# Optimization experiments

Hardware: AMD Instinct MI355X
Metric: run time of the kernel (lower is better)

Reference implementation:

```python
import jax, jax.numpy as jnp
import numpy as np

N = 100000
E = 1600000
F_IN = 602
NHID = 128
N_CLS = 41


def setup_inputs() -> dict:
    key = jax.random.key(0)
    k1, k2, k3, k4 = jax.random.split(key, 4)
    x = jax.random.normal(k1, (N, F_IN), dtype=jnp.float32)
    edge_index = jax.random.randint(k2, (2, E), 0, N, dtype=jnp.int64)
    # Glorot-style scaled weights
    W1 = jax.random.normal(k3, (F_IN, NHID), dtype=jnp.float32) * (1.0 / np.sqrt(F_IN))
    b1 = jnp.zeros((NHID,), dtype=jnp.float32)
    W2 = jax.random.normal(k4, (NHID, N_CLS), dtype=jnp.float32) * (1.0 / np.sqrt(NHID))
    b2 = jnp.zeros((N_CLS,), dtype=jnp.float32)
    return {"x": x, "edge_index": edge_index, "W1": W1, "b1": b1, "W2": W2, "b2": b2}


def reference(x, edge_index, W1, b1, W2, b2):
    n = x.shape[0]
    loop = jnp.arange(n, dtype=edge_index.dtype)
    # PyG GCNConv: add self-loops, symmetric normalization D^-1/2 (A+I) D^-1/2
    src = jnp.concatenate([edge_index[0], loop])  # [E+N]
    dst = jnp.concatenate([edge_index[1], loop])  # [E+N]
    ones = jnp.ones(src.shape[0], dtype=x.dtype)
    deg = jax.ops.segment_sum(ones, dst, num_segments=n)  # in-degree incl self-loop
    dinv = jnp.where(deg > 0, jax.lax.rsqrt(deg), 0.0)
    norm = dinv[src] * dinv[dst]  # [E+N]

    def conv(h, W, b):
        h = h @ W  # transform first (smaller feature dim for gather)
        msg = h[src] * norm[:, None]  # gather + scale
        return jax.ops.segment_sum(msg, dst, num_segments=n) + b  # scatter-add

    h = jax.nn.relu(conv(x, W1, b1))
    # dropout is identity in eval mode
    out = conv(h, W2, b2)
    return jax.nn.log_softmax(out, axis=1)
```

## Files before the change

kernel.cpp:

```cpp
#include <hip/hip_runtime.h>
#include <math.h>

#define GK 602
#define GH 128
#define GC 41
#define GCP 48
#define KPAD 608
#define NKT 19
#define GS 40

typedef __bf16 bf16x8 __attribute__((ext_vector_type(8)));
typedef float f32x16 __attribute__((ext_vector_type(16)));

__device__ __forceinline__ unsigned short f2bf(float f) {
    __bf16 b = (__bf16)f;
    return __builtin_bit_cast(unsigned short, b);
}
__device__ __forceinline__ float bf2f(unsigned short u) {
    return __uint_as_float((unsigned int)u << 16);
}
__device__ __forceinline__ float bflo(unsigned int u) { return __uint_as_float(u << 16); }
__device__ __forceinline__ float bfhi(unsigned int u) { return __uint_as_float(u & 0xffff0000u); }


__global__ void k_hist(const int* __restrict__ dst, int* __restrict__ counts, int E) {
    int e = blockIdx.x * 256 + threadIdx.x;
    if (e < E) atomicAdd(&counts[dst[e]], 1);
}

__global__ void k_scan_a(const int* __restrict__ counts, int* __restrict__ row_ptr,
                         int* __restrict__ bsum, int n) {
    __shared__ int wsum[4];
    int t = threadIdx.x;
    int lane = t & 63;
    int wv = t >> 6;
    int base = blockIdx.x * 1024 + t * 4;
    int v[4];
    int s = 0;
#pragma unroll
    for (int j = 0; j < 4; ++j) {
        int idx = base + j;
        v[j] = (idx < n) ? counts[idx] : 0;
        s += v[j];
    }
    int incl = s;
#pragma unroll
    for (int o = 1; o < 64; o <<= 1) {
        int x = __shfl_up(incl, o);
        if (lane >= o) incl += x;
    }
    if (lane == 63) wsum[wv] = incl;
    __syncthreads();
    int woff = 0;
#pragma unroll
    for (int i = 0; i < 3; ++i) woff += (i < wv) ? wsum[i] : 0;
    if (t == 255) bsum[blockIdx.x] = woff + incl;
    int off = woff + incl - s;
#pragma unroll
    for (int j = 0; j < 4; ++j) {
        int idx = base + j;
        if (idx < n) row_ptr[idx] = off;
        off += v[j];
    }
}

__global__ void k_scan_b(int* __restrict__ bsum, int nb) {
    __shared__ int sh[256];
    int t = threadIdx.x;
    int v = (t < nb) ? bsum[t] : 0;
    sh[t] = v;
    __syncthreads();
    for (int o = 1; o < 256; o <<= 1) {
        int x = (t >= o) ? sh[t - o] : 0;
        __syncthreads();
        sh[t] += x;
        __syncthreads();
    }
    if (t < nb) bsum[t] = sh[t] - v;
}

__global__ void k_scan_c(int* __restrict__ row_ptr, const int* __restrict__ bsum,
                         const int* __restrict__ counts, float* __restrict__ dinv,
                         int* __restrict__ cursor, int n, int E) {
    int i = blockIdx.x * 256 + threadIdx.x;
    if (i < n) {
        int rp = row_ptr[i] + bsum[i >> 10];
        row_ptr[i] = rp;
        cursor[i] = rp;
        dinv[i] = rsqrtf((float)(counts[i] + 1));
    }
    if (i == 0) row_ptr[n] = E;
}

__global__ void k_fill(const int* __restrict__ src, const int* __restrict__ dst,
                       const float* __restrict__ dinv,
                       int* __restrict__ cursor, int2* __restrict__ meta, int E) {
    int e = blockIdx.x * 256 + threadIdx.x;
    if (e < E) {
        int s = src[e];
        int d = dst[e];
        int p = atomicAdd(&cursor[d], 1);
        float w = dinv[s] * dinv[d];
        meta[p] = make_int2(s, __float_as_int(w));
    }
}


__global__ void k_prepW1(const float* __restrict__ W1, unsigned short* __restrict__ W1T) {
    int i = blockIdx.x * 256 + threadIdx.x;
    if (i >= GH * KPAD) return;
    int n = i / KPAD;
    int k = i - n * KPAD;
    float v = (k < GK) ? W1[(size_t)k * GH + n] : 0.f;
    W1T[i] = f2bf(v);
}


struct AF { float4 v0, v1, v2, v3; };

__device__ __forceinline__ AF loadA(const float* __restrict__ xr, int kb, bool tail) {
    AF r;
    if (!tail) {
        r.v0 = *(const float4*)(xr + kb);
        r.v1 = *(const float4*)(xr + kb + 4);
        r.v2 = *(const float4*)(xr + kb + 16);
        r.v3 = *(const float4*)(xr + kb + 20);
    } else {
        float tv[8], tw[8];
#pragma unroll
        for (int j = 0; j < 8; ++j) {
            int k0_ = kb + j;
            int k1_ = kb + 16 + j;
            tv[j] = (k0_ < GK) ? xr[k0_] : 0.f;
            tw[j] = (k1_ < GK) ? xr[k1_] : 0.f;
        }
        r.v0 = make_float4(tv[0], tv[1], tv[2], tv[3]);
        r.v1 = make_float4(tv[4], tv[5], tv[6], tv[7]);
        r.v2 = make_float4(tw[0], tw[1], tw[2], tw[3]);
        r.v3 = make_float4(tw[4], tw[5], tw[6], tw[7]);
    }
    return r;
}

__device__ __forceinline__ bf16x8 cvt8(float4 a, float4 b) {
    bf16x8 r;
    r[0] = (__bf16)a.x; r[1] = (__bf16)a.y; r[2] = (__bf16)a.z; r[3] = (__bf16)a.w;
    r[4] = (__bf16)b.x; r[5] = (__bf16)b.y; r[6] = (__bf16)b.z; r[7] = (__bf16)b.w;
    return r;
}

__device__ __forceinline__ void stageB(const unsigned short* __restrict__ W1T,
                                       __bf16* __restrict__ Bsb, int tid, int k0) {
#pragma unroll
    for (int s = 0; s < 2; ++s) {
        int slot = tid + 256 * s;
        int n = slot >> 2;
        int j = slot & 3;
        uint4 v = *(const uint4*)&W1T[(size_t)n * KPAD + k0 + 8 * j];
        *(uint4*)&Bsb[n * GS + 8 * j] = v;
    }
}

__global__ __launch_bounds__(256) void k_gemm1_mfma(const float* __restrict__ X,
                                                    const unsigned short* __restrict__ W1T,
                                                    unsigned short* __restrict__ Y, int M) {
    __shared__ __bf16 Bs[2][128 * GS];
    int tid = threadIdx.x;
    int lane = tid & 63;
    int w = tid >> 6;
    int rowBase = blockIdx.x * 64 + (w & 1) * 32;
    int cg = w >> 1;
    int grow_base = rowBase + (lane & 31);
    int arow = (grow_base < M) ? grow_base : (M - 1);
    const float* xr = X + (size_t)arow * GK;
    int kh = (lane >> 5) * 8;
    int bn = lane & 31;

    f32x16 acc[2];
#pragma unroll
    for (int c = 0; c < 2; ++c)
#pragma unroll
        for (int i = 0; i < 16; ++i) acc[c][i] = 0.f;

    stageB(W1T, Bs[0], tid, 0);
    AF a = loadA(xr, kh, false);
    __syncthreads();

    int buf = 0;
    for (int it = 0; it < NKT; ++it) {
        AF an;
        if (it + 1 < NKT) {
            stageB(W1T, Bs[buf ^ 1], tid, 32 * (it + 1));
            an = loadA(xr, kh + 32 * (it + 1), (it + 1) == (NKT - 1));
        }
        bf16x8 af0 = cvt8(a.v0, a.v1);
        bf16x8 af1 = cvt8(a.v2, a.v3);
#pragma unroll
        for (int c = 0; c < 2; ++c) {
            int nt = 2 * cg + c;
            bf16x8 b0 = *(const bf16x8*)&Bs[buf][(32 * nt + bn) * GS + kh];
            acc[c] = __builtin_amdgcn_mfma_f32_32x32x16_bf16(af0, b0, acc[c], 0, 0, 0);
        }
#pragma unroll
        for (int c = 0; c < 2; ++c) {
            int nt = 2 * cg + c;
            bf16x8 b1 = *(const bf16x8*)&Bs[buf][(32 * nt + bn) * GS + 16 + kh];
            acc[c] = __builtin_amdgcn_mfma_f32_32x32x16_bf16(af1, b1, acc[c], 0, 0, 0);
        }
        __syncthreads();
        buf ^= 1;
        a = an;
    }
#pragma unroll
    for (int c = 0; c < 2; ++c) {
        int nt = 2 * cg + c;
#pragma unroll
        for (int reg = 0; reg < 16; ++reg) {
            int rrow = (reg & 3) + 8 * (reg >> 2) + 4 * (lane >> 5);
            int grow = rowBase + rrow;
            int gcol = 32 * nt + (lane & 31);
            if (grow < M) Y[(size_t)grow * GH + gcol] = f2bf(acc[c][reg]);
        }
    }
}


__global__ __launch_bounds__(256) void k_agg1(const unsigned int* __restrict__ H,
                                              unsigned int* __restrict__ O,
                                              const int* __restrict__ row_ptr,
                                              const int2* __restrict__ meta,
                                              const float* __restrict__ dinv,
                                              const float* __restrict__ bias, int n) {
    int wv = threadIdx.x >> 6;
    int lane = threadIdx.x & 63;
    int d = blockIdx.x * 4 + wv;
    if (d >= n) return;
    float dd = dinv[d];
    int beg = row_ptr[d], end = row_ptr[d + 1];
    unsigned int v = H[(size_t)d * 64 + lane];
    float sw = dd * dd;
    float a0 = sw * bflo(v);
    float a1 = sw * bfhi(v);
    int e = beg;
    for (; e + 16 <= end; e += 16) {
        int2 m[16];
        unsigned int u[16];
#pragma unroll
        for (int j = 0; j < 16; ++j) m[j] = meta[e + j];
#pragma unroll
        for (int j = 0; j < 16; ++j) u[j] = H[(size_t)m[j].x * 64 + lane];
#pragma unroll
        for (int j = 0; j < 16; ++j) {
            float wj = __int_as_float(m[j].y);
            a0 = fmaf(wj, bflo(u[j]), a0);
            a1 = fmaf(wj, bfhi(u[j]), a1);
        }
    }
    if (e + 8 <= end) {
        int2 m[8];
        unsigned int u[8];
#pragma unroll
        for (int j = 0; j < 8; ++j) m[j] = meta[e + j];
#pragma unroll
        for (int j = 0; j < 8; ++j) u[j] = H[(size_t)m[j].x * 64 + lane];
#pragma unroll
        for (int j = 0; j < 8; ++j) {
            float wj = __int_as_float(m[j].y);
            a0 = fmaf(wj, bflo(u[j]), a0);
            a1 = fmaf(wj, bfhi(u[j]), a1);
        }
        e += 8;
    }
    if (e + 4 <= end) {
        int2 m[4];
        unsigned int u[4];
#pragma unroll
        for (int j = 0; j < 4; ++j) m[j] = meta[e + j];
#pragma unroll
        for (int j = 0; j < 4; ++j) u[j] = H[(size_t)m[j].x * 64 + lane];
#pragma unroll
        for (int j = 0; j < 4; ++j) {
            float wj = __int_as_float(m[j].y);
            a0 = fmaf(wj, bflo(u[j]), a0);
            a1 = fmaf(wj, bfhi(u[j]), a1);
        }
        e += 4;
    }
    for (; e < end; ++e) {
        int2 m = meta[e];
        unsigned int u = H[(size_t)m.x * 64 + lane];
        float wj = __int_as_float(m.y);
        a0 = fmaf(wj, bflo(u), a0);
        a1 = fmaf(wj, bfhi(u), a1);
    }
    a0 = fmaxf(a0 + bias[2 * lane], 0.f);
    a1 = fmaxf(a1 + bias[2 * lane + 1], 0.f);
    O[(size_t)d * 64 + lane] = (unsigned int)f2bf(a0) | ((unsigned int)f2bf(a1) << 16);
}


__global__ __launch_bounds__(256) void k_gemm2t(const unsigned int* __restrict__ Hb,
                                                const float* __restrict__ W2,
                                                unsigned short* __restrict__ G, int n) {
    __shared__ float ws[128][GCP];
    for (int i = threadIdx.x; i < 128 * GCP; i += 256) {
        int k = i / GCP;
        int c = i - k * GCP;
        ws[k][c] = (c < GC) ? W2[k * GC + c] : 0.f;
    }
    __syncthreads();
    int r0 = blockIdx.x * 512 + threadIdx.x;
    int r1 = r0 + 256;
    bool v0 = r0 < n, v1 = r1 < n;
    float acc0[GCP], acc1[GCP];
#pragma unroll
    for (int c = 0; c < GCP; ++c) { acc0[c] = 0.f; acc1[c] = 0.f; }
    const uint2* h0 = (const uint2*)(Hb + (size_t)(v0 ? r0 : 0) * 64);
    const uint2* h1 = (const uint2*)(Hb + (size_t)(v1 ? r1 : 0) * 64);
    for (int q = 0; q < 32; ++q) {
        uint2 ua = h0[q];
        uint2 ub = h1[q];
        float va[4] = {bflo(ua.x), bfhi(ua.x), bflo(ua.y), bfhi(ua.y)};
        float vb[4] = {bflo(ub.x), bfhi(ub.x), bflo(ub.y), bfhi(ub.y)};
#pragma unroll
        for (int j = 0; j < 4; ++j) {
            int k = 4 * q + j;
#pragma unroll
            for (int cq = 0; cq < GCP / 4; ++cq) {
                float4 wv = *(const float4*)&ws[k][4 * cq];
                acc0[4 * cq + 0] = fmaf(va[j], wv.x, acc0[4 * cq + 0]);
                acc0[4 * cq + 1] = fmaf(va[j], wv.y, acc0[4 * cq + 1]);
                acc0[4 * cq + 2] = fmaf(va[j], wv.z, acc0[4 * cq + 2]);
                acc0[4 * cq + 3] = fmaf(va[j], wv.w, acc0[4 * cq + 3]);
                acc1[4 * cq + 0] = fmaf(vb[j], wv.x, acc1[4 * cq + 0]);
                acc1[4 * cq + 1] = fmaf(vb[j], wv.y, acc1[4 * cq + 1]);
                acc1[4 * cq + 2] = fmaf(vb[j], wv.z, acc1[4 * cq + 2]);
                acc1[4 * cq + 3] = fmaf(vb[j], wv.w, acc1[4 * cq + 3]);
            }
        }
    }
    if (v0) {
#pragma unroll
        for (int c = 0; c < GCP; ++c) G[(size_t)r0 * GCP + c] = f2bf(acc0[c]);
    }
    if (v1) {
#pragma unroll
        for (int c = 0; c < GCP; ++c) G[(size_t)r1 * GCP + c] = f2bf(acc1[c]);
    }
}


__global__ __launch_bounds__(256) void k_agg2(const unsigned short* __restrict__ G,
                                              float* __restrict__ out,
                                              const int* __restrict__ row_ptr,
                                              const int2* __restrict__ meta,
                                              const float* __restrict__ dinv,
                                              const float* __restrict__ b2, int n) {
    int wv = threadIdx.x >> 6;
    int lane = threadIdx.x & 63;
    int gl = (lane < GCP) ? lane : (GCP - 1);
    int d = blockIdx.x * 4 + wv;
    if (d >= n) return;
    float dd = dinv[d];
    int beg = row_ptr[d], end = row_ptr[d + 1];
    float a = dd * dd * bf2f(G[(size_t)d * GCP + gl]);
    int e = beg;
    for (; e + 16 <= end; e += 16) {
        int2 m[16];
        unsigned short u[16];
#pragma unroll
        for (int j = 0; j < 16; ++j) m[j] = meta[e + j];
#pragma unroll
        for (int j = 0; j < 16; ++j) u[j] = G[(size_t)m[j].x * GCP + gl];
#pragma unroll
        for (int j = 0; j < 16; ++j) a = fmaf(__int_as_float(m[j].y), bf2f(u[j]), a);
    }
    if (e + 8 <= end) {
        int2 m[8];
        unsigned short u[8];
#pragma unroll
        for (int j = 0; j < 8; ++j) m[j] = meta[e + j];
#pragma unroll
        for (int j = 0; j < 8; ++j) u[j] = G[(size_t)m[j].x * GCP + gl];
#pragma unroll
        for (int j = 0; j < 8; ++j) a = fmaf(__int_as_float(m[j].y), bf2f(u[j]), a);
        e += 8;
    }
    if (e + 4 <= end) {
        int2 m[4];
        unsigned short u[4];
#pragma unroll
        for (int j = 0; j < 4; ++j) m[j] = meta[e + j];
#pragma unroll
        for (int j = 0; j < 4; ++j) u[j] = G[(size_t)m[j].x * GCP + gl];
#pragma unroll
        for (int j = 0; j < 4; ++j) a = fmaf(__int_as_float(m[j].y), bf2f(u[j]), a);
        e += 4;
    }
    for (; e < end; ++e) {
        int2 m = meta[e];
        a = fmaf(__int_as_float(m.y), bf2f(G[(size_t)m.x * GCP + gl]), a);
    }
    float logit = (lane < GC) ? (a + b2[lane]) : -INFINITY;
    float mx = logit;
#pragma unroll
    for (int off = 32; off; off >>= 1) mx = fmaxf(mx, __shfl_xor(mx, off));
    float ex = (lane < GC) ? __expf(logit - mx) : 0.f;
    float sm = ex;
#pragma unroll
    for (int off = 32; off; off >>= 1) sm += __shfl_xor(sm, off);
    if (lane < GC) out[(size_t)d * GC + lane] = logit - mx - __logf(sm);
}


static inline size_t alignup256(size_t x) { return (x + 255) & ~(size_t)255; }

extern "C" void kernel_launch(void* const* d_in, const int* in_sizes, int n_in,
                              void* d_out, int out_size, void* d_ws, size_t ws_size,
                              hipStream_t stream) {
    const float* x  = (const float*)d_in[0];
    const int*   ei = (const int*)d_in[1];
    const float* W1 = (const float*)d_in[2];
    const float* b1 = (const float*)d_in[3];
    const float* W2 = (const float*)d_in[4];
    const float* b2 = (const float*)d_in[5];
    float* out = (float*)d_out;

    const int n = in_sizes[0] / GK;
    const int E = in_sizes[1] / 2;
    const int* src = ei;
    const int* dst = ei + E;

    char* w = (char*)d_ws;
    char* p;
    p = w; w += alignup256((size_t)n * 4);            float* dinv  = (float*)p;
    p = w; w += alignup256((size_t)n * 4);            int* counts  = (int*)p;
    p = w; w += alignup256((size_t)n * 4);            int* cursor  = (int*)p;
    p = w; w += alignup256((size_t)(n + 1) * 4);      int* row_ptr = (int*)p;
    p = w; w += alignup256(1024 * 4);                 int* bsum    = (int*)p;
    p = w; w += alignup256((size_t)E * 8);            int2* meta   = (int2*)p;
    p = w; w += alignup256((size_t)GH * KPAD * 2);    unsigned short* W1T = (unsigned short*)p;
    p = w; w += alignup256((size_t)n * GH * 2);       unsigned short* bufA = (unsigned short*)p;
    p = w; w += alignup256((size_t)n * GH * 2);       unsigned short* bufB = (unsigned short*)p;
    p = w; w += alignup256((size_t)n * GCP * 2);      unsigned short* G    = (unsigned short*)p;

    hipMemsetAsync(counts, 0, (size_t)n * 4, stream);

    int gE = (E + 255) / 256;
    int gN = (n + 255) / 256;
    int nb = (n + 1023) / 1024;

    k_hist<<<gE, 256, 0, stream>>>(dst, counts, E);
    k_scan_a<<<nb, 256, 0, stream>>>(counts, row_ptr, bsum, n);
    k_scan_b<<<1, 256, 0, stream>>>(bsum, nb);
    k_scan_c<<<gN, 256, 0, stream>>>(row_ptr, bsum, counts, dinv, cursor, n, E);
    k_fill<<<gE, 256, 0, stream>>>(src, dst, dinv, cursor, meta, E);

    k_prepW1<<<(GH * KPAD + 255) / 256, 256, 0, stream>>>(W1, W1T);
    k_gemm1_mfma<<<(n + 63) / 64, 256, 0, stream>>>(x, W1T, bufA, n);
    k_agg1<<<(n + 3) / 4, 256, 0, stream>>>((const unsigned int*)bufA, (unsigned int*)bufB,
                                            row_ptr, meta, dinv, b1, n);
    k_gemm2t<<<(n + 511) / 512, 256, 0, stream>>>((const unsigned int*)bufB, W2, G, n);
    k_agg2<<<(n + 3) / 4, 256, 0, stream>>>(G, out, row_ptr, meta, dinv, b2, n);
}
```

Before: 721.7 us.

## Restructure GEMM1: per-wave 32x128 tiles, fragment-packed W1 from global, LDS-staged coalesced X

The first-layer GEMM is reorganised so each wave computes a full 32-row by 128-column tile, making four MFMA accumulators and 128 rows per block. W1 is pre-packed into MFMA fragment order, so B operands are read straight from global memory (L2/L1-resident) instead of being staged through shared memory with barriers. X rows are loaded with coalesced float4 reads, converted to bf16 and written to a per-wave double-buffered LDS region, with no block-level syncs. The goal is to cut redundant X reads, LDS traffic and barrier stalls in the memory-bound X stream. In exchange it adds register pressure and depends on cache hits for the W1 fragments.

```diff
diff --git a/kernel.cpp b/kernel.cpp
--- a/kernel.cpp
+++ b/kernel.cpp
@@ -7,7 +7,6 @@
 #define GCP 48
 #define KPAD 608
 #define NKT 19
-#define GS 40
 
 typedef __bf16 bf16x8 __attribute__((ext_vector_type(8)));
 typedef float f32x16 __attribute__((ext_vector_type(16)));
@@ -106,122 +105,126 @@
 }
 
 
-__global__ void k_prepW1(const float* __restrict__ W1, unsigned short* __restrict__ W1T) {
+__global__ void k_prepW1F(const float* __restrict__ W1, unsigned short* __restrict__ W1F) {
     int i = blockIdx.x * 256 + threadIdx.x;
-    if (i >= GH * KPAD) return;
-    int n = i / KPAD;
-    int k = i - n * KPAD;
-    float v = (k < GK) ? W1[(size_t)k * GH + n] : 0.f;
-    W1T[i] = f2bf(v);
-}
-
-
-struct AF { float4 v0, v1, v2, v3; };
-
-__device__ __forceinline__ AF loadA(const float* __restrict__ xr, int kb, bool tail) {
-    AF r;
-    if (!tail) {
-        r.v0 = *(const float4*)(xr + kb);
-        r.v1 = *(const float4*)(xr + kb + 4);
-        r.v2 = *(const float4*)(xr + kb + 16);
-        r.v3 = *(const float4*)(xr + kb + 20);
-    } else {
-        float tv[8], tw[8];
-#pragma unroll
-        for (int j = 0; j < 8; ++j) {
-            int k0_ = kb + j;
-            int k1_ = kb + 16 + j;
-            tv[j] = (k0_ < GK) ? xr[k0_] : 0.f;
-            tw[j] = (k1_ < GK) ? xr[k1_] : 0.f;
-        }
-        r.v0 = make_float4(tv[0], tv[1], tv[2], tv[3]);
-        r.v1 = make_float4(tv[4], tv[5], tv[6], tv[7]);
-        r.v2 = make_float4(tw[0], tw[1], tw[2], tw[3]);
-        r.v3 = make_float4(tw[4], tw[5], tw[6], tw[7]);
-    }
-    return r;
-}
-
-__device__ __forceinline__ bf16x8 cvt8(float4 a, float4 b) {
-    bf16x8 r;
-    r[0] = (__bf16)a.x; r[1] = (__bf16)a.y; r[2] = (__bf16)a.z; r[3] = (__bf16)a.w;
-    r[4] = (__bf16)b.x; r[5] = (__bf16)b.y; r[6] = (__bf16)b.z; r[7] = (__bf16)b.w;
-    return r;
-}
-
-__device__ __forceinline__ void stageB(const unsigned short* __restrict__ W1T,
-                                       __bf16* __restrict__ Bsb, int tid, int k0) {
-#pragma unroll
-    for (int s = 0; s < 2; ++s) {
-        int slot = tid + 256 * s;
-        int n = slot >> 2;
-        int j = slot & 3;
-        uint4 v = *(const uint4*)&W1T[(size_t)n * KPAD + k0 + 8 * j];
-        *(uint4*)&Bsb[n * GS + 8 * j] = v;
-    }
-}
-
-__global__ __launch_bounds__(256) void k_gemm1_mfma(const float* __restrict__ X,
-                                                    const unsigned short* __restrict__ W1T,
-                                                    unsigned short* __restrict__ Y, int M) {
-    __shared__ __bf16 Bs[2][128 * GS];
+    if (i >= NKT * 4096) return;
+    int kt = i >> 12;
+    int r  = i & 4095;
+    int nt = r >> 10;
+    int r2 = r & 1023;
+    int bs = r2 >> 9;
+    int r3 = r2 & 511;
+    int ln = r3 >> 3;
+    int j  = r3 & 7;
+    int col = 32 * nt + (ln & 31);
+    int k   = 32 * kt + 16 * bs + 8 * (ln >> 5) + j;
+    float v = (k < GK) ? W1[(size_t)k * GH + col] : 0.f;
+    W1F[i] = f2bf(v);
+}
+
+
+__device__ __forceinline__ void issueA(const float* __restrict__ X, int rowBase,
+                                       int ro, int q, int kb, int M, float4* av) {
+#pragma unroll
+    for (int i = 0; i < 4; ++i) {
+        int r = rowBase + 8 * i + ro;
+        if (r >= M) r = M - 1;
+        const float* p = X + (size_t)r * GK + kb + 4 * q;
+        av[i] = *(const float4*)p;
+    }
+}
+
+__device__ __forceinline__ void issueA_tail(const float* __restrict__ X, int rowBase,
+                                            int ro, int q, int kb, int M, float4* av) {
+#pragma unroll
+    for (int i = 0; i < 4; ++i) {
+        int r = rowBase + 8 * i + ro;
+        if (r >= M) r = M - 1;
+        const float* p = X + (size_t)r * GK;
+        int k0 = kb + 4 * q;
+        float t0 = (k0 + 0 < GK) ? p[k0 + 0] : 0.f;
+        float t1 = (k0 + 1 < GK) ? p[k0 + 1] : 0.f;
+        float t2 = (k0 + 2 < GK) ? p[k0 + 2] : 0.f;
+        float t3 = (k0 + 3 < GK) ? p[k0 + 3] : 0.f;
+        av[i] = make_float4(t0, t1, t2, t3);
+    }
+}
+
+__device__ __forceinline__ void writeA(unsigned short* __restrict__ As, int wbase,
+                                       int ro, int q, const float4* av) {
+    int af   = q >> 2;
+    int half = (q >> 1) & 1;
+    int bo   = (q & 1) * 4;
+#pragma unroll
+    for (int i = 0; i < 4; ++i) {
+        int d = 8 * i + ro + 32 * half;
+        unsigned short* p = As + wbase + af * 512 + d * 8 + bo;
+        ushort4 h;
+        h.x = f2bf(av[i].x);
+        h.y = f2bf(av[i].y);
+        h.z = f2bf(av[i].z);
+        h.w = f2bf(av[i].w);
+        *(ushort4*)p = h;
+    }
+}
+
+__global__ __launch_bounds__(256, 3) void k_gemm1_mfma(const float* __restrict__ X,
+                                                       const unsigned short* __restrict__ W1F,
+                                                       unsigned short* __restrict__ Y, int M) {
+    __shared__ unsigned short As[8192];
     int tid = threadIdx.x;
     int lane = tid & 63;
     int w = tid >> 6;
-    int rowBase = blockIdx.x * 64 + (w & 1) * 32;
-    int cg = w >> 1;
-    int grow_base = rowBase + (lane & 31);
-    int arow = (grow_base < M) ? grow_base : (M - 1);
-    const float* xr = X + (size_t)arow * GK;
-    int kh = (lane >> 5) * 8;
-    int bn = lane & 31;
-
-    f32x16 acc[2];
-#pragma unroll
-    for (int c = 0; c < 2; ++c)
+    int rowBase = blockIdx.x * 128 + w * 32;
+    int ro = lane >> 3;
+    int q  = lane & 7;
+
+    f32x16 acc[4];
+#pragma unroll
+    for (int c = 0; c < 4; ++c)
 #pragma unroll
         for (int i = 0; i < 16; ++i) acc[c][i] = 0.f;
 
-    stageB(W1T, Bs[0], tid, 0);
-    AF a = loadA(xr, kh, false);
-    __syncthreads();
-
-    int buf = 0;
-    for (int it = 0; it < NKT; ++it) {
-        AF an;
-        if (it + 1 < NKT) {
-            stageB(W1T, Bs[buf ^ 1], tid, 32 * (it + 1));
-            an = loadA(xr, kh + 32 * (it + 1), (it + 1) == (NKT - 1));
-        }
-        bf16x8 af0 = cvt8(a.v0, a.v1);
-        bf16x8 af1 = cvt8(a.v2, a.v3);
-#pragma unroll
-        for (int c = 0; c < 2; ++c) {
-            int nt = 2 * cg + c;
-            bf16x8 b0 = *(const bf16x8*)&Bs[buf][(32 * nt + bn) * GS + kh];
-            acc[c] = __builtin_amdgcn_mfma_f32_32x32x16_bf16(af0, b0, acc[c], 0, 0, 0);
-        }
-#pragma unroll
-        for (int c = 0; c < 2; ++c) {
-            int nt = 2 * cg + c;
-            bf16x8 b1 = *(const bf16x8*)&Bs[buf][(32 * nt + bn) * GS + 16 + kh];
-            acc[c] = __builtin_amdgcn_mfma_f32_32x32x16_bf16(af1, b1, acc[c], 0, 0, 0);
-        }
-        __syncthreads();
-        buf ^= 1;
-        a = an;
-    }
-#pragma unroll
-    for (int c = 0; c < 2; ++c) {
-        int nt = 2 * cg + c;
+    const unsigned short* Wb = W1F + lane * 8;
+    int wbase0 = w * 2048;
+
+    float4 av[4];
+    issueA(X, rowBase, ro, q, 0, M, av);
+    writeA(As, wbase0, ro, q, av);
+
+    for (int t = 0; t < NKT; ++t) {
+        int buf = t & 1;
+        float4 nv[4];
+        if (t + 1 < NKT) {
+            if (t + 1 == NKT - 1) issueA_tail(X, rowBase, ro, q, 32 * (t + 1), M, nv);
+            else                  issueA(X, rowBase, ro, q, 32 * (t + 1), M, nv);
+        }
+        const unsigned short* Asw = As + wbase0 + buf * 1024;
+        bf16x8 a0 = *(const bf16x8*)(Asw + lane * 8);
+        bf16x8 a1 = *(const bf16x8*)(Asw + 512 + lane * 8);
+        const unsigned short* Wt = Wb + t * 4096;
+#pragma unroll
+        for (int c = 0; c < 4; ++c) {
+            bf16x8 b0 = *(const bf16x8*)(Wt + c * 1024);
+            acc[c] = __builtin_amdgcn_mfma_f32_32x32x16_bf16(a0, b0, acc[c], 0, 0, 0);
+        }
+#pragma unroll
+        for (int c = 0; c < 4; ++c) {
+            bf16x8 b1 = *(const bf16x8*)(Wt + c * 1024 + 512);
+            acc[c] = __builtin_amdgcn_mfma_f32_32x32x16_bf16(a1, b1, acc[c], 0, 0, 0);
+        }
+        if (t + 1 < NKT) writeA(As, wbase0 + (buf ^ 1) * 1024, ro, q, nv);
+    }
+
+#pragma unroll
+    for (int c = 0; c < 4; ++c)
 #pragma unroll
         for (int reg = 0; reg < 16; ++reg) {
             int rrow = (reg & 3) + 8 * (reg >> 2) + 4 * (lane >> 5);
             int grow = rowBase + rrow;
-            int gcol = 32 * nt + (lane & 31);
+            int gcol = 32 * c + (lane & 31);
             if (grow < M) Y[(size_t)grow * GH + gcol] = f2bf(acc[c][reg]);
         }
-    }
 }
 
 
@@ -439,7 +442,7 @@
     p = w; w += alignup256((size_t)(n + 1) * 4);      int* row_ptr = (int*)p;
     p = w; w += alignup256(1024 * 4);                 int* bsum    = (int*)p;
     p = w; w += alignup256((size_t)E * 8);            int2* meta   = (int2*)p;
-    p = w; w += alignup256((size_t)GH * KPAD * 2);    unsigned short* W1T = (unsigned short*)p;
+    p = w; w += alignup256((size_t)GH * KPAD * 2);    unsigned short* W1F = (unsigned short*)p;
     p = w; w += alignup256((size_t)n * GH * 2);       unsigned short* bufA = (unsigned short*)p;
     p = w; w += alignup256((size_t)n * GH * 2);       unsigned short* bufB = (unsigned short*)p;
     p = w; w += alignup256((size_t)n * GCP * 2);      unsigned short* G    = (unsigned short*)p;
@@ -456,8 +459,8 @@
     k_scan_c<<<gN, 256, 0, stream>>>(row_ptr, bsum, counts, dinv, cursor, n, E);
     k_fill<<<gE, 256, 0, stream>>>(src, dst, dinv, cursor, meta, E);
 
-    k_prepW1<<<(GH * KPAD + 255) / 256, 256, 0, stream>>>(W1, W1T);
-    k_gemm1_mfma<<<(n + 63) / 64, 256, 0, stream>>>(x, W1T, bufA, n);
+    k_prepW1F<<<(NKT * 4096 + 255) / 256, 256, 0, stream>>>(W1, W1F);
+    k_gemm1_mfma<<<(n + 127) / 128, 256, 0, stream>>>(x, W1F, bufA, n);
     k_agg1<<<(n + 3) / 4, 256, 0, stream>>>((const unsigned int*)bufA, (unsigned int*)bufB,
                                             row_ptr, meta, dinv, b1, n);
     k_gemm2t<<<(n + 511) / 512, 256, 0, stream>>>((const unsigned int*)bufB, W2, G, n);
```

Measured after the change: 742.4 us. +2.9%, slower.

## Pre-swizzle W1 into MFMA fragment layout and load B directly from global

Applied to the files above, without the earlier changes.

W1 is now repacked on the device into the exact per-lane MFMA B-fragment order, so the GEMM kernel loads B operands straight from global/L2 memory instead of staging them through double-buffered LDS with block barriers. The A prefetch is deepened to two k-tiles ahead, and launch bounds now request 4 blocks per CU. This removes LDS traffic and the per-iteration __syncthreads. In exchange, every wave re-reads W1 from cache, and the extra A registers may raise register pressure.

```diff
diff --git a/kernel.cpp b/kernel.cpp
--- a/kernel.cpp
+++ b/kernel.cpp
@@ -7,7 +7,6 @@
 #define GCP 48
 #define KPAD 608
 #define NKT 19
-#define GS 40
 
 typedef __bf16 bf16x8 __attribute__((ext_vector_type(8)));
 typedef float f32x16 __attribute__((ext_vector_type(16)));
@@ -106,13 +105,21 @@
 }
 
 
-__global__ void k_prepW1(const float* __restrict__ W1, unsigned short* __restrict__ W1T) {
+__global__ void k_prepW1F(const float* __restrict__ W1, unsigned short* __restrict__ W1F) {
     int i = blockIdx.x * 256 + threadIdx.x;
-    if (i >= GH * KPAD) return;
-    int n = i / KPAD;
-    int k = i - n * KPAD;
-    float v = (k < GK) ? W1[(size_t)k * GH + n] : 0.f;
-    W1T[i] = f2bf(v);
+    if (i >= NKT * 4096) return;
+    int kt = i >> 12;
+    int r  = i & 4095;
+    int nt = r >> 10;
+    int r2 = r & 1023;
+    int bs = r2 >> 9;
+    int r3 = r2 & 511;
+    int ln = r3 >> 3;
+    int j  = r3 & 7;
+    int col = 32 * nt + (ln & 31);
+    int k   = 32 * kt + 16 * bs + 8 * (ln >> 5) + j;
+    float v = (k < GK) ? W1[(size_t)k * GH + col] : 0.f;
+    W1F[i] = f2bf(v);
 }
 
 
@@ -149,22 +156,9 @@
     return r;
 }
 
-__device__ __forceinline__ void stageB(const unsigned short* __restrict__ W1T,
-                                       __bf16* __restrict__ Bsb, int tid, int k0) {
-#pragma unroll
-    for (int s = 0; s < 2; ++s) {
-        int slot = tid + 256 * s;
-        int n = slot >> 2;
-        int j = slot & 3;
-        uint4 v = *(const uint4*)&W1T[(size_t)n * KPAD + k0 + 8 * j];
-        *(uint4*)&Bsb[n * GS + 8 * j] = v;
-    }
-}
-
-__global__ __launch_bounds__(256) void k_gemm1_mfma(const float* __restrict__ X,
-                                                    const unsigned short* __restrict__ W1T,
-                                                    unsigned short* __restrict__ Y, int M) {
-    __shared__ __bf16 Bs[2][128 * GS];
+__global__ __launch_bounds__(256, 4) void k_gemm1_mfma(const float* __restrict__ X,
+                                                       const unsigned short* __restrict__ W1F,
+                                                       unsigned short* __restrict__ Y, int M) {
     int tid = threadIdx.x;
     int lane = tid & 63;
     int w = tid >> 6;
@@ -174,7 +168,6 @@
     int arow = (grow_base < M) ? grow_base : (M - 1);
     const float* xr = X + (size_t)arow * GK;
     int kh = (lane >> 5) * 8;
-    int bn = lane & 31;
 
     f32x16 acc[2];
 #pragma unroll
@@ -182,35 +175,34 @@
 #pragma unroll
         for (int i = 0; i < 16; ++i) acc[c][i] = 0.f;
 
-    stageB(W1T, Bs[0], tid, 0);
-    AF a = loadA(xr, kh, false);
-    __syncthreads();
-
-    int buf = 0;
-    for (int it = 0; it < NKT; ++it) {
-        AF an;
-        if (it + 1 < NKT) {
-            stageB(W1T, Bs[buf ^ 1], tid, 32 * (it + 1));
-            an = loadA(xr, kh + 32 * (it + 1), (it + 1) == (NKT - 1));
-        }
-        bf16x8 af0 = cvt8(a.v0, a.v1);
-        bf16x8 af1 = cvt8(a.v2, a.v3);
-#pragma unroll
-        for (int c = 0; c < 2; ++c) {
-            int nt = 2 * cg + c;
-            bf16x8 b0 = *(const bf16x8*)&Bs[buf][(32 * nt + bn) * GS + kh];
-            acc[c] = __builtin_amdgcn_mfma_f32_32x32x16_bf16(af0, b0, acc[c], 0, 0, 0);
-        }
-#pragma unroll
-        for (int c = 0; c < 2; ++c) {
-            int nt = 2 * cg + c;
-            bf16x8 b1 = *(const bf16x8*)&Bs[buf][(32 * nt + bn) * GS + 16 + kh];
-            acc[c] = __builtin_amdgcn_mfma_f32_32x32x16_bf16(af1, b1, acc[c], 0, 0, 0);
-        }
-        __syncthreads();
-        buf ^= 1;
-        a = an;
-    }
+    const unsigned short* Wb = W1F + (size_t)lane * 8 + (size_t)cg * 2048;
+
+    AF a0 = loadA(xr, kh, false);
+    AF a1 = loadA(xr, kh + 32, false);
+
+    for (int t = 0; t < NKT; ++t) {
+        AF a2;
+        if (t + 2 < NKT) a2 = loadA(xr, kh + 32 * (t + 2), (t + 2) == (NKT - 1));
+        else             a2 = a1;
+
+        const unsigned short* Wt = Wb + (size_t)t * 4096;
+        bf16x8 af0 = cvt8(a0.v0, a0.v1);
+        bf16x8 af1 = cvt8(a0.v2, a0.v3);
+
+        bf16x8 b00 = *(const bf16x8*)(Wt);
+        bf16x8 b10 = *(const bf16x8*)(Wt + 1024);
+        acc[0] = __builtin_amdgcn_mfma_f32_32x32x16_bf16(af0, b00, acc[0], 0, 0, 0);
+        acc[1] = __builtin_amdgcn_mfma_f32_32x32x16_bf16(af0, b10, acc[1], 0, 0, 0);
+
+        bf16x8 b01 = *(const bf16x8*)(Wt + 512);
+        bf16x8 b11 = *(const bf16x8*)(Wt + 1024 + 512);
+        acc[0] = __builtin_amdgcn_mfma_f32_32x32x16_bf16(af1, b01, acc[0], 0, 0, 0);
+        acc[1] = __builtin_amdgcn_mfma_f32_32x32x16_bf16(af1, b11, acc[1], 0, 0, 0);
+
+        a0 = a1;
+        a1 = a2;
+    }
+
 #pragma unroll
     for (int c = 0; c < 2; ++c) {
         int nt = 2 * cg + c;
@@ -439,7 +431,7 @@
     p = w; w += alignup256((size_t)(n + 1) * 4);      int* row_ptr = (int*)p;
     p = w; w += alignup256(1024 * 4);                 int* bsum    = (int*)p;
     p = w; w += alignup256((size_t)E * 8);            int2* meta   = (int2*)p;
-    p = w; w += alignup256((size_t)GH * KPAD * 2);    unsigned short* W1T = (unsigned short*)p;
+    p = w; w += alignup256((size_t)GH * KPAD * 2);    unsigned short* W1F = (unsigned short*)p;
     p = w; w += alignup256((size_t)n * GH * 2);       unsigned short* bufA = (unsigned short*)p;
     p = w; w += alignup256((size_t)n * GH * 2);       unsigned short* bufB = (unsigned short*)p;
     p = w; w += alignup256((size_t)n * GCP * 2);      unsigned short* G    = (unsigned short*)p;
@@ -456,8 +448,8 @@
     k_scan_c<<<gN, 256, 0, stream>>>(row_ptr, bsum, counts, dinv, cursor, n, E);
     k_fill<<<gE, 256, 0, stream>>>(src, dst, dinv, cursor, meta, E);
 
-    k_prepW1<<<(GH * KPAD + 255) / 256, 256, 0, stream>>>(W1, W1T);
-    k_gemm1_mfma<<<(n + 63) / 64, 256, 0, stream>>>(x, W1T, bufA, n);
+    k_prepW1F<<<(NKT * 4096 + 255) / 256, 256, 0, stream>>>(W1, W1F);
+    k_gemm1_mfma<<<(n + 63) / 64, 256, 0, stream>>>(x, W1F, bufA, n);
     k_agg1<<<(n + 3) / 4, 256, 0, stream>>>((const unsigned int*)bufA, (unsigned int*)bufB,
                                             row_ptr, meta, dinv, b1, n);
     k_gemm2t<<<(n + 511) / 512, 256, 0, stream>>>((const unsigned int*)bufB, W2, G, n);
```

Result: slower. 758.8 us (+5.1%).
